# Optimization experiments

Measured on AMD Instinct MI355X. Metric: run time of the kernel, lower is better.

## Reference

```python
import jax, jax.numpy as jnp
import numpy as np

NUM_E = 100000
NUM_R = 500
HIDDEN = 64
BATCH = 32
GAMMA = 12.0
EPSILON = 2.0
EMB_RANGE = (GAMMA + EPSILON) / HIDDEN  # 0.21875
PI = 3.141592653589793


def setup_inputs() -> dict:
    key = jax.random.key(0)
    k1, k2, k3 = jax.random.split(key, 3)
    facts = jax.random.randint(k1, (BATCH, 3), 0, 1000, dtype=jnp.int64)  # col0<num_e, col1<2*num_r
    entity_embedding = jax.random.uniform(
        k2, (NUM_E, 2 * HIDDEN), dtype=jnp.float32, minval=-EMB_RANGE, maxval=EMB_RANGE)
    relation_embedding = jax.random.uniform(
        k3, (NUM_R * 2, HIDDEN), dtype=jnp.float32, minval=-EMB_RANGE, maxval=EMB_RANGE)
    return {"facts": facts, "entity_embedding": entity_embedding,
            "relation_embedding": relation_embedding}


def reference(facts, entity_embedding, relation_embedding):
    # Gather head/relation embeddings for the batch
    head = entity_embedding[facts[:, 0]]          # [B, 2D]
    relation = relation_embedding[facts[:, 1]]    # [B, D]

    re_head, im_head = jnp.split(head, 2, axis=1)           # [B, D] each
    re_tail, im_tail = jnp.split(entity_embedding, 2, axis=1)  # [E, D] each

    phase = relation / (EMB_RANGE / PI)
    re_rel = jnp.cos(phase)
    im_rel = jnp.sin(phase)

    # Complex rotation of head by relation: [B, D]
    re_rot = re_head * re_rel - im_head * im_rel
    im_rot = re_head * im_rel + im_head * re_rel

    # Broadcast difference against all entities: [B, E, D]
    re_diff = re_rot[:, None, :] - re_tail[None, :, :]
    im_diff = im_rot[:, None, :] - im_tail[None, :, :]

    # Per-component complex modulus, summed over dim -> [B, E]
    dist = jnp.sqrt(re_diff * re_diff + im_diff * im_diff).sum(axis=2)
    return GAMMA - dist
```

## Files before the change

kernel.cpp:

```cpp
#include <hip/hip_runtime.h>
#include <math.h>

#define NUM_E   100000
#define HIDDEN  64
#define BATCH   32
#define GAMMA_F 12.0f
#define EMB_RANGE_F 0.21875f
#define INV_TWO_EMB (1.0f / (2.0f * EMB_RANGE_F))

typedef float v4f __attribute__((ext_vector_type(4)));
typedef float v2f __attribute__((ext_vector_type(2)));

static __device__ __forceinline__ v2f pk_sub(v2f a, v2f b) {
    v2f d;
    asm("v_pk_add_f32 %0, %1, %2 neg_lo:[0,1] neg_hi:[0,1]"
        : "=v"(d) : "v"(a), "v"(b));
    return d;
}
static __device__ __forceinline__ v2f pk_mul(v2f a, v2f b) {
    v2f d;
    asm("v_pk_mul_f32 %0, %1, %2" : "=v"(d) : "v"(a), "v"(b));
    return d;
}
static __device__ __forceinline__ v2f pk_fma(v2f a, v2f b, v2f c) {
    v2f d;
    asm("v_pk_fma_f32 %0, %1, %2, %3" : "=v"(d) : "v"(a), "v"(b), "v"(c));
    return d;
}
static __device__ __forceinline__ float sq2(v2f dx, v2f dy) {
    v2f sq = pk_fma(dy, dy, pk_mul(dx, dx));
    return __builtin_amdgcn_sqrtf(sq.x) + __builtin_amdgcn_sqrtf(sq.y);
}
static __device__ __forceinline__ v2f lo2(v4f v) { return __builtin_shufflevector(v, v, 0, 1); }
static __device__ __forceinline__ v2f hi2(v4f v) { return __builtin_shufflevector(v, v, 2, 3); }

template <int CTRL>
static __device__ __forceinline__ float dpp_xor_add(float x) {
    int y = __builtin_amdgcn_update_dpp(0, __float_as_int(x), CTRL, 0xF, 0xF, true);
    return x + __int_as_float(y);
}

__global__ void rotate_phase_kernel(const int* __restrict__ facts,
                                    const float* __restrict__ ent,
                                    const float* __restrict__ rel,
                                    float* __restrict__ rot) {
    int p = blockIdx.x * blockDim.x + threadIdx.x;
    if (p >= BATCH * HIDDEN) return;
    int b = p >> 6;
    int d = p & 63;
    int f0 = facts[b * 3 + 0];
    int f1 = facts[b * 3 + 1];
    float hre = ent[(size_t)f0 * 128 + d];
    float him = ent[(size_t)f0 * 128 + 64 + d];
    float r   = rel[(size_t)f1 * 64 + d];
    float rev = r * INV_TWO_EMB;
    float s = __builtin_amdgcn_sinf(rev);
    float c = __builtin_amdgcn_cosf(rev);
    rot[p]                  = hre * c - him * s;
    rot[BATCH * HIDDEN + p] = hre * s + him * c;
}

__global__ __launch_bounds__(256, 4) void rotate_dist_kernel(
        const float* __restrict__ ent,
        const float* __restrict__ rot,
        float* __restrict__ out) {
    __shared__ float s_ent[4096];
    __shared__ float s_scr[4][136];

    const int t    = threadIdx.x;
    const int lane = t & 63;
    const int wv   = t >> 6;
    const int bg   = lane >> 3;
    const int dg   = lane & 7;
    const int e0   = blockIdx.x * 32 + wv * 8;

    v2f RR[4][4], RI[4][4];
#pragma unroll
    for (int kb = 0; kb < 4; ++kb) {
        const v4f* pr = (const v4f*)(rot + (bg * 4 + kb) * 64 + dg * 8);
        const v4f* pi = (const v4f*)(rot + 2048 + (bg * 4 + kb) * 64 + dg * 8);
        v4f a = pr[0], b = pr[1], c = pi[0], d = pi[1];
        RR[kb][0] = lo2(a); RR[kb][1] = hi2(a); RR[kb][2] = lo2(b); RR[kb][3] = hi2(b);
        RI[kb][0] = lo2(c); RI[kb][1] = hi2(c); RI[kb][2] = lo2(d); RI[kb][3] = hi2(d);
    }

    float* lds = s_ent + wv * 1024;
    {
        const v4f* g4 = (const v4f*)(ent + (size_t)e0 * 128);
        v4f* s4 = (v4f*)lds;
#pragma unroll
        for (int k = 0; k < 4; ++k) s4[k * 64 + lane] = g4[k * 64 + lane];
    }

    float* scr = s_scr[wv];

#pragma unroll 1
    for (int grp = 0; grp < 2; ++grp) {
        float p[4][4];

#pragma unroll
        for (int i = 0; i < 4; ++i) {
            const float* base = lds + (grp * 4 + i) * 128 + dg * 8;
            v4f er0 = *(const v4f*)(base);
            v4f er1 = *(const v4f*)(base + 4);
            v4f ei0 = *(const v4f*)(base + 64);
            v4f ei1 = *(const v4f*)(base + 68);
            v2f e2[4] = { lo2(er0), hi2(er0), lo2(er1), hi2(er1) };
            v2f i2[4] = { lo2(ei0), hi2(ei0), lo2(ei1), hi2(ei1) };
#pragma unroll
            for (int kb = 0; kb < 4; ++kb) {
                float s0 = sq2(pk_sub(RR[kb][0], e2[0]), pk_sub(RI[kb][0], i2[0]));
                float s1 = sq2(pk_sub(RR[kb][1], e2[1]), pk_sub(RI[kb][1], i2[1]));
                float s2 = sq2(pk_sub(RR[kb][2], e2[2]), pk_sub(RI[kb][2], i2[2]));
                float s3 = sq2(pk_sub(RR[kb][3], e2[3]), pk_sub(RI[kb][3], i2[3]));
                p[i][kb] = (s0 + s1) + (s2 + s3);
            }
        }

#pragma unroll
        for (int i = 0; i < 4; ++i)
#pragma unroll
            for (int kb = 0; kb < 4; ++kb) {
                float v = p[i][kb];
                v = dpp_xor_add<0xB1>(v);
                v = dpp_xor_add<0x4E>(v);
                v += __shfl_xor(v, 4, 64);
                p[i][kb] = GAMMA_F - v;
            }

        if (dg < 4) {
#pragma unroll
            for (int i = 0; i < 4; ++i) {
                float val = (dg == 0) ? p[i][0] : (dg == 1) ? p[i][1]
                          : (dg == 2) ? p[i][2] : p[i][3];
                scr[i * 33 + bg * 4 + dg] = val;
            }
        }
#pragma unroll
        for (int j = 0; j < 2; ++j) {
            const int b  = (lane >> 2) + 16 * j;
            const int el = lane & 3;
            float v = scr[el * 33 + b];
            out[(size_t)b * NUM_E + e0 + grp * 4 + el] = v;
        }
    }
}

extern "C" void kernel_launch(void* const* d_in, const int* in_sizes, int n_in,
                              void* d_out, int out_size, void* d_ws, size_t ws_size,
                              hipStream_t stream) {
    const int*   facts = (const int*)d_in[0];
    const float* ent   = (const float*)d_in[1];
    const float* rel   = (const float*)d_in[2];
    float*       out   = (float*)d_out;
    float*       rot   = (float*)d_ws;

    rotate_phase_kernel<<<dim3((BATCH * HIDDEN + 255) / 256), dim3(256), 0, stream>>>(
        facts, ent, rel, rot);

    rotate_dist_kernel<<<dim3(NUM_E / 32), dim3(256), 0, stream>>>(
        ent, rot, out);
}
```

Baseline: 119.5 us.

## Fuse rotation prologue into persistent distance kernel with register prefetch

Removes the separate phase-rotation kernel: each wave now computes its rotated head vectors directly from facts and the embedding tables (recomputing sin/cos per wave). The distance kernel becomes persistent, with 1024 blocks where each wave strides over entities one at a time, and the next entity row is prefetched into registers instead of being staged through LDS. Each entity's 32 outputs are written straight to global memory as scattered 4-byte stores, dropping the LDS transpose. The aim is to save a kernel launch and LDS traffic, at the cost of redundant prologue work and less coalesced output stores.

```diff
diff --git a/kernel.cpp b/kernel.cpp
--- a/kernel.cpp
+++ b/kernel.cpp
@@ -2,11 +2,12 @@
 #include <math.h>
 
 #define NUM_E   100000
-#define HIDDEN  64
-#define BATCH   32
 #define GAMMA_F 12.0f
 #define EMB_RANGE_F 0.21875f
 #define INV_TWO_EMB (1.0f / (2.0f * EMB_RANGE_F))
+
+#define NBLK  1024
+#define NWAVE (NBLK * 4)
 
 typedef float v4f __attribute__((ext_vector_type(4)));
 typedef float v2f __attribute__((ext_vector_type(2)));
@@ -40,108 +41,90 @@
     return x + __int_as_float(y);
 }
 
-__global__ void rotate_phase_kernel(const int* __restrict__ facts,
-                                    const float* __restrict__ ent,
-                                    const float* __restrict__ rel,
-                                    float* __restrict__ rot) {
-    int p = blockIdx.x * blockDim.x + threadIdx.x;
-    if (p >= BATCH * HIDDEN) return;
-    int b = p >> 6;
-    int d = p & 63;
-    int f0 = facts[b * 3 + 0];
-    int f1 = facts[b * 3 + 1];
-    float hre = ent[(size_t)f0 * 128 + d];
-    float him = ent[(size_t)f0 * 128 + 64 + d];
-    float r   = rel[(size_t)f1 * 64 + d];
-    float rev = r * INV_TWO_EMB;
-    float s = __builtin_amdgcn_sinf(rev);
-    float c = __builtin_amdgcn_cosf(rev);
-    rot[p]                  = hre * c - him * s;
-    rot[BATCH * HIDDEN + p] = hre * s + him * c;
-}
-
-__global__ __launch_bounds__(256, 4) void rotate_dist_kernel(
+__global__ __launch_bounds__(256, 4) void rotate_dist_fused(
+        const int*   __restrict__ facts,
         const float* __restrict__ ent,
-        const float* __restrict__ rot,
-        float* __restrict__ out) {
-    __shared__ float s_ent[4096];
-    __shared__ float s_scr[4][136];
-
+        const float* __restrict__ rel,
+        float*       __restrict__ out) {
     const int t    = threadIdx.x;
     const int lane = t & 63;
     const int wv   = t >> 6;
     const int bg   = lane >> 3;
     const int dg   = lane & 7;
-    const int e0   = blockIdx.x * 32 + wv * 8;
+    const int wid  = blockIdx.x * 4 + wv;
 
     v2f RR[4][4], RI[4][4];
 #pragma unroll
     for (int kb = 0; kb < 4; ++kb) {
-        const v4f* pr = (const v4f*)(rot + (bg * 4 + kb) * 64 + dg * 8);
-        const v4f* pi = (const v4f*)(rot + 2048 + (bg * 4 + kb) * 64 + dg * 8);
-        v4f a = pr[0], b = pr[1], c = pi[0], d = pi[1];
-        RR[kb][0] = lo2(a); RR[kb][1] = hi2(a); RR[kb][2] = lo2(b); RR[kb][3] = hi2(b);
-        RI[kb][0] = lo2(c); RI[kb][1] = hi2(c); RI[kb][2] = lo2(d); RI[kb][3] = hi2(d);
+        const int b  = bg * 4 + kb;
+        const int f0 = facts[b * 3 + 0];
+        const int f1 = facts[b * 3 + 1];
+        const float* hp = ent + (size_t)f0 * 128 + dg * 8;
+        const float* rp = rel + (size_t)f1 * 64  + dg * 8;
+        float hre[8], him[8], ph[8];
+        *(v4f*)&hre[0] = *(const v4f*)(hp);
+        *(v4f*)&hre[4] = *(const v4f*)(hp + 4);
+        *(v4f*)&him[0] = *(const v4f*)(hp + 64);
+        *(v4f*)&him[4] = *(const v4f*)(hp + 68);
+        *(v4f*)&ph[0]  = *(const v4f*)(rp);
+        *(v4f*)&ph[4]  = *(const v4f*)(rp + 4);
+        float rer[8], imr[8];
+#pragma unroll
+        for (int j = 0; j < 8; ++j) {
+            float rev = ph[j] * INV_TWO_EMB;
+            float s = __builtin_amdgcn_sinf(rev);
+            float c = __builtin_amdgcn_cosf(rev);
+            rer[j] = hre[j] * c - him[j] * s;
+            imr[j] = hre[j] * s + him[j] * c;
+        }
+#pragma unroll
+        for (int j = 0; j < 4; ++j) {
+            RR[kb][j] = (v2f){rer[2 * j], rer[2 * j + 1]};
+            RI[kb][j] = (v2f){imr[2 * j], imr[2 * j + 1]};
+        }
     }
 
-    float* lds = s_ent + wv * 1024;
+    float* obase = out + (size_t)(bg * 4 + (dg & 3)) * NUM_E;
+
+    int e = wid;
     {
-        const v4f* g4 = (const v4f*)(ent + (size_t)e0 * 128);
-        v4f* s4 = (v4f*)lds;
-#pragma unroll
-        for (int k = 0; k < 4; ++k) s4[k * 64 + lane] = g4[k * 64 + lane];
-    }
+        const float* ep = ent + (size_t)e * 128 + dg * 8;
+        v4f er0 = *(const v4f*)(ep);
+        v4f er1 = *(const v4f*)(ep + 4);
+        v4f ei0 = *(const v4f*)(ep + 64);
+        v4f ei1 = *(const v4f*)(ep + 68);
 
-    float* scr = s_scr[wv];
+        while (e < NUM_E) {
+            const int en = e + NWAVE;
+            const int ec = (en < NUM_E) ? en : e;
+            const float* np = ent + (size_t)ec * 128 + dg * 8;
+            v4f nr0 = *(const v4f*)(np);
+            v4f nr1 = *(const v4f*)(np + 4);
+            v4f ni0 = *(const v4f*)(np + 64);
+            v4f ni1 = *(const v4f*)(np + 68);
 
-#pragma unroll 1
-    for (int grp = 0; grp < 2; ++grp) {
-        float p[4][4];
-
-#pragma unroll
-        for (int i = 0; i < 4; ++i) {
-            const float* base = lds + (grp * 4 + i) * 128 + dg * 8;
-            v4f er0 = *(const v4f*)(base);
-            v4f er1 = *(const v4f*)(base + 4);
-            v4f ei0 = *(const v4f*)(base + 64);
-            v4f ei1 = *(const v4f*)(base + 68);
             v2f e2[4] = { lo2(er0), hi2(er0), lo2(er1), hi2(er1) };
             v2f i2[4] = { lo2(ei0), hi2(ei0), lo2(ei1), hi2(ei1) };
+            float r[4];
 #pragma unroll
             for (int kb = 0; kb < 4; ++kb) {
                 float s0 = sq2(pk_sub(RR[kb][0], e2[0]), pk_sub(RI[kb][0], i2[0]));
                 float s1 = sq2(pk_sub(RR[kb][1], e2[1]), pk_sub(RI[kb][1], i2[1]));
                 float s2 = sq2(pk_sub(RR[kb][2], e2[2]), pk_sub(RI[kb][2], i2[2]));
                 float s3 = sq2(pk_sub(RR[kb][3], e2[3]), pk_sub(RI[kb][3], i2[3]));
-                p[i][kb] = (s0 + s1) + (s2 + s3);
-            }
-        }
-
-#pragma unroll
-        for (int i = 0; i < 4; ++i)
-#pragma unroll
-            for (int kb = 0; kb < 4; ++kb) {
-                float v = p[i][kb];
+                float v = (s0 + s1) + (s2 + s3);
                 v = dpp_xor_add<0xB1>(v);
                 v = dpp_xor_add<0x4E>(v);
                 v += __shfl_xor(v, 4, 64);
-                p[i][kb] = GAMMA_F - v;
+                r[kb] = GAMMA_F - v;
             }
-
-        if (dg < 4) {
-#pragma unroll
-            for (int i = 0; i < 4; ++i) {
-                float val = (dg == 0) ? p[i][0] : (dg == 1) ? p[i][1]
-                          : (dg == 2) ? p[i][2] : p[i][3];
-                scr[i * 33 + bg * 4 + dg] = val;
+            if (dg < 4) {
+                float val = (dg == 0) ? r[0] : (dg == 1) ? r[1]
+                          : (dg == 2) ? r[2] : r[3];
+                obase[e] = val;
             }
-        }
-#pragma unroll
-        for (int j = 0; j < 2; ++j) {
-            const int b  = (lane >> 2) + 16 * j;
-            const int el = lane & 3;
-            float v = scr[el * 33 + b];
-            out[(size_t)b * NUM_E + e0 + grp * 4 + el] = v;
+            er0 = nr0; er1 = nr1; ei0 = ni0; ei1 = ni1;
+            e = en;
         }
     }
 }
@@ -153,11 +136,7 @@
     const float* ent   = (const float*)d_in[1];
     const float* rel   = (const float*)d_in[2];
     float*       out   = (float*)d_out;
-    float*       rot   = (float*)d_ws;
+    (void)d_ws; (void)ws_size;
 
-    rotate_phase_kernel<<<dim3((BATCH * HIDDEN + 255) / 256), dim3(256), 0, stream>>>(
-        facts, ent, rel, rot);
-
-    rotate_dist_kernel<<<dim3(NUM_E / 32), dim3(256), 0, stream>>>(
-        ent, rot, out);
+    rotate_dist_fused<<<dim3(NBLK), dim3(256), 0, stream>>>(facts, ent, rel, out);
 }
```

After: 144.7 us. 21.1% more time.
